# Performance work log

Hardware: AMD Instinct MI355X
Metric: run time of the kernel (lower is better)

The kernel has to match this reference:

```python
import jax, jax.numpy as jnp
import numpy as np

N_EMBD = 1024
N_HEAD = 16
HEAD_DIM = N_EMBD // N_HEAD
EPS = 1e-5


def _gelu_tanh(x):
    c = jnp.sqrt(jnp.asarray(2.0 / jnp.pi, x.dtype))
    return 0.5 * x * (1.0 + jnp.tanh(c * (x + 0.044715 * x ** 3)))


def _layernorm(x, scale, shift):
    # torch.var defaults to unbiased (ddof=1) -- replicate exactly
    mean = jnp.mean(x, axis=-1, keepdims=True)
    var = jnp.var(x, axis=-1, keepdims=True, ddof=1)
    return (x - mean) / jnp.sqrt(var + EPS) * scale + shift


def setup_inputs() -> dict:
    key = jax.random.key(0)
    ks = jax.random.split(key, 8)
    d, h = N_EMBD, 4 * N_EMBD
    s = 0.02
    return {
        "x": jax.random.normal(ks[0], (2, 2048, d), jnp.float32),
        "ln1_scale": jnp.ones((d,), jnp.float32),
        "ln1_shift": jnp.zeros((d,), jnp.float32),
        "wq": jax.random.normal(ks[1], (d, d), jnp.float32) * s,
        "wk": jax.random.normal(ks[2], (d, d), jnp.float32) * s,
        "wv": jax.random.normal(ks[3], (d, d), jnp.float32) * s,
        "w_out": jax.random.normal(ks[4], (d, d), jnp.float32) * s,
        "b_out": jnp.zeros((d,), jnp.float32),
        "ln2_scale": jnp.ones((d,), jnp.float32),
        "ln2_shift": jnp.zeros((d,), jnp.float32),
        "w1": jax.random.normal(ks[5], (d, h), jnp.float32) * s,
        "b1": jnp.zeros((h,), jnp.float32),
        "w2": jax.random.normal(ks[6], (h, d), jnp.float32) * s,
        "b2": jnp.zeros((d,), jnp.float32),
    }


def reference(x, ln1_scale, ln1_shift, wq, wk, wv, w_out, b_out,
              ln2_scale, ln2_shift, w1, b1, w2, b2):
    B, S, D = x.shape
    out = _layernorm(x, ln1_scale, ln1_shift)

    # qkv projections (no bias), split heads: [B, H, S, hd]
    q = (out @ wq).reshape(B, S, N_HEAD, HEAD_DIM).transpose(0, 2, 1, 3)
    k = (out @ wk).reshape(B, S, N_HEAD, HEAD_DIM).transpose(0, 2, 1, 3)
    v = (out @ wv).reshape(B, S, N_HEAD, HEAD_DIM).transpose(0, 2, 1, 3)

    scores = jnp.einsum("bhqd,bhkd->bhqk", q, k)
    causal = jnp.triu(jnp.ones((S, S), bool), k=1)
    # original masks BEFORE scaling; -inf / sqrt(d) is still -inf
    scores = jnp.where(causal, -jnp.inf, scores)
    weights = jax.nn.softmax(scores / jnp.sqrt(jnp.asarray(HEAD_DIM, scores.dtype)), axis=-1)
    ctx = jnp.einsum("bhqk,bhkd->bqhd", weights, v).reshape(B, S, D)
    attn_out = ctx @ w_out + b_out

    out = attn_out + x  # dropout is identity (rate 0)
    shortcut = out
    out = _layernorm(out, ln2_scale, ln2_shift)
    out = _gelu_tanh(out @ w1 + b1) @ w2 + b2
    return out + shortcut
```

## Files before the change

### kernel.cpp

```cpp
#include <hip/hip_runtime.h>
#include <stdint.h>
#include <math.h>

using bf16x8 = __attribute__((ext_vector_type(8))) short;
using f32x4  = __attribute__((ext_vector_type(4))) float;

__device__ __forceinline__ uint16_t f2b(float f) {
    union { float f; uint32_t i; } v; v.f = f;
    uint32_t r = v.i + 0x7fffu + ((v.i >> 16) & 1u);
    return (uint16_t)(r >> 16);
}
__device__ __forceinline__ float b2f(uint16_t u) {
    union { uint32_t i; float f; } v; v.i = ((uint32_t)u) << 16; return v.f;
}

typedef const __attribute__((address_space(1))) void gvoid;
typedef __attribute__((address_space(3))) void svoid;

__global__ __launch_bounds__(256) void fill_zero(float* __restrict__ o, int n) {
    int i = (blockIdx.x * 256 + threadIdx.x) * 4;
    if (i < n) *(float4*)(o + i) = make_float4(0.f, 0.f, 0.f, 0.f);
}

__global__ __launch_bounds__(256) void transpose_qkvo(
    const float* __restrict__ wq, const float* __restrict__ wk,
    const float* __restrict__ wv, const float* __restrict__ wo,
    uint16_t* __restrict__ wqkvT, uint16_t* __restrict__ woT)
{
    const int D = 1024;
    int z = blockIdx.z;
    const float* W = (z == 0) ? wq : (z == 1) ? wk : (z == 2) ? wv : wo;
    uint16_t* Wt = (z < 3) ? (wqkvT + (size_t)z * D * D) : woT;
    __shared__ uint16_t t[32][33];
    int n0 = blockIdx.x * 32, k0 = blockIdx.y * 32;
    int tx = threadIdx.x, ty = threadIdx.y;
    #pragma unroll
    for (int i = ty; i < 32; i += 8)
        t[i][tx] = f2b(W[(size_t)(k0 + i) * D + (n0 + tx)]);
    __syncthreads();
    #pragma unroll
    for (int i = ty; i < 32; i += 8)
        Wt[(size_t)(n0 + i) * D + (k0 + tx)] = t[tx][i];
}

__global__ __launch_bounds__(256) void transpose_f2b(
    const float* __restrict__ W, uint16_t* __restrict__ Wt, int K, int N)
{
    __shared__ uint16_t t[32][33];
    int n0 = blockIdx.x * 32, k0 = blockIdx.y * 32;
    int tx = threadIdx.x, ty = threadIdx.y;
    #pragma unroll
    for (int i = ty; i < 32; i += 8)
        t[i][tx] = f2b(W[(size_t)(k0 + i) * N + (n0 + tx)]);
    __syncthreads();
    #pragma unroll
    for (int i = ty; i < 32; i += 8)
        Wt[(size_t)(n0 + i) * K + (k0 + tx)] = t[tx][i];
}

__global__ __launch_bounds__(256) void ln_kernel(
    const float* __restrict__ src, const float* __restrict__ scale,
    const float* __restrict__ shift, uint16_t* __restrict__ out)
{
    const int D = 1024;
    int row = blockIdx.x, t = threadIdx.x;
    float4 f = *((const float4*)(src + (size_t)row * D) + t);
    float v[4] = {f.x, f.y, f.z, f.w};
    float s1 = v[0] + v[1] + v[2] + v[3];
    float s2 = v[0]*v[0] + v[1]*v[1] + v[2]*v[2] + v[3]*v[3];
    #pragma unroll
    for (int off = 32; off; off >>= 1) {
        s1 += __shfl_xor(s1, off);
        s2 += __shfl_xor(s2, off);
    }
    __shared__ float red[2][4];
    __shared__ float stat[2];
    int wid = t >> 6, lane = t & 63;
    if (lane == 0) { red[0][wid] = s1; red[1][wid] = s2; }
    __syncthreads();
    if (t == 0) {
        float S1 = red[0][0] + red[0][1] + red[0][2] + red[0][3];
        float S2 = red[1][0] + red[1][1] + red[1][2] + red[1][3];
        float mean = S1 / (float)D;
        float var  = fmaxf((S2 - mean * S1) / (float)(D - 1), 0.f);
        stat[0] = mean; stat[1] = rsqrtf(var + 1e-5f);
    }
    __syncthreads();
    float mean = stat[0], rstd = stat[1];
    float4 sc = *((const float4*)scale + t);
    float4 sh = *((const float4*)shift + t);
    uint16_t o[4];
    o[0] = f2b((v[0] - mean) * rstd * sc.x + sh.x);
    o[1] = f2b((v[1] - mean) * rstd * sc.y + sh.y);
    o[2] = f2b((v[2] - mean) * rstd * sc.z + sh.z);
    o[3] = f2b((v[3] - mean) * rstd * sc.w + sh.w);
    uint2 st;
    st.x = (uint32_t)o[0] | ((uint32_t)o[1] << 16);
    st.y = (uint32_t)o[2] | ((uint32_t)o[3] << 16);
    *(uint2*)(out + (size_t)row * D + t * 4) = st;
}

__global__ __launch_bounds__(256) void combine2(
    float* __restrict__ dst, const float* __restrict__ part0,
    const float* __restrict__ resid, const float* __restrict__ bias)
{
    const int D = 1024;
    size_t o = (size_t)blockIdx.x * D + threadIdx.x * 4;
    float4 a = *(float4*)(dst + o);
    float4 b = *(const float4*)(part0 + o);
    float4 c = *(const float4*)(resid + o);
    float4 bv = *((const float4*)bias + threadIdx.x);
    a.x += b.x + c.x + bv.x;
    a.y += b.y + c.y + bv.y;
    a.z += b.z + c.z + bv.z;
    a.w += b.w + c.w + bv.w;
    *(float4*)(dst + o) = a;
}

__global__ __launch_bounds__(256) void combine2ln(
    float* __restrict__ res1, const float* __restrict__ part0,
    const float* __restrict__ x, const float* __restrict__ bo,
    const float* __restrict__ scale, const float* __restrict__ shift,
    uint16_t* __restrict__ out)
{
    const int D = 1024;
    int row = blockIdx.x, t = threadIdx.x;
    size_t o = (size_t)row * D + t * 4;
    float4 a = *(float4*)(res1 + o);
    float4 b = *(const float4*)(part0 + o);
    float4 c = *(const float4*)(x + o);
    float4 bv = *((const float4*)bo + t);
    float v[4] = {a.x + b.x + c.x + bv.x, a.y + b.y + c.y + bv.y,
                  a.z + b.z + c.z + bv.z, a.w + b.w + c.w + bv.w};
    *(float4*)(res1 + o) = make_float4(v[0], v[1], v[2], v[3]);

    float s1 = v[0] + v[1] + v[2] + v[3];
    float s2 = v[0]*v[0] + v[1]*v[1] + v[2]*v[2] + v[3]*v[3];
    #pragma unroll
    for (int off = 32; off; off >>= 1) {
        s1 += __shfl_xor(s1, off);
        s2 += __shfl_xor(s2, off);
    }
    __shared__ float red[2][4];
    __shared__ float stat[2];
    int wid = t >> 6, lane = t & 63;
    if (lane == 0) { red[0][wid] = s1; red[1][wid] = s2; }
    __syncthreads();
    if (t == 0) {
        float S1 = red[0][0] + red[0][1] + red[0][2] + red[0][3];
        float S2 = red[1][0] + red[1][1] + red[1][2] + red[1][3];
        float mean = S1 / (float)D;
        float var  = fmaxf((S2 - mean * S1) / (float)(D - 1), 0.f);
        stat[0] = mean; stat[1] = rsqrtf(var + 1e-5f);
    }
    __syncthreads();
    float mean = stat[0], rstd = stat[1];
    float4 sc = *((const float4*)scale + t);
    float4 sh = *((const float4*)shift + t);
    uint16_t ob[4];
    ob[0] = f2b((v[0] - mean) * rstd * sc.x + sh.x);
    ob[1] = f2b((v[1] - mean) * rstd * sc.y + sh.y);
    ob[2] = f2b((v[2] - mean) * rstd * sc.z + sh.z);
    ob[3] = f2b((v[3] - mean) * rstd * sc.w + sh.w);
    uint2 st;
    st.x = (uint32_t)ob[0] | ((uint32_t)ob[1] << 16);
    st.y = (uint32_t)ob[2] | ((uint32_t)ob[3] << 16);
    *(uint2*)(out + (size_t)row * D + t * 4) = st;
}

template <int EPI>
__global__ __launch_bounds__(256) void gemm128(
    const uint16_t* __restrict__ A, const uint16_t* __restrict__ Bt,
    const float* __restrict__ bias, const float* __restrict__ resid,
    void* __restrict__ outp, void* __restrict__ out2,
    int M, int N, int K, int lda)
{
    __shared__ __align__(16) uint16_t As[2][128 * 32];
    __shared__ __align__(16) uint16_t Bs[2][128 * 32];
    int tid = threadIdx.x;
    int w = tid >> 6, l = tid & 63;
    int quad = l >> 4, ln = l & 15;

    int Nt = gridDim.x, Mt = gridDim.y;
    int L0 = blockIdx.y * Nt + blockIdx.x;
    int nb = Nt * Mt;
    int L = (L0 & 7) * (nb >> 3) + (L0 >> 3);
    const int GROUP = 8;
    int nig = GROUP * Nt;
    int gid = L / nig;
    int fm = gid * GROUP;
    int gsz = min(Mt - fm, GROUP);
    int rem = L - gid * nig;
    int pid_m = fm + rem % gsz;
    int pid_n = rem / gsz;
    int n0 = pid_n * 128, m0 = pid_m * 128;
    int kofs = (EPI == 5) ? blockIdx.z * K : 0;

    int mo = (w & 1) * 64, no = (w >> 1) * 64;
    int srow = l >> 2;
    int scol = (l & 3) * 8;

    f32x4 acc[4][4];
    #pragma unroll
    for (int mi = 0; mi < 4; ++mi)
        #pragma unroll
        for (int ni = 0; ni < 4; ++ni) acc[mi][ni] = (f32x4){0.f, 0.f, 0.f, 0.f};

    for (int k0 = 0; k0 < K; k0 += 64) {
        __syncthreads();
        #pragma unroll
        for (int p = 0; p < 2; ++p) {
            int arow = p * 64 + w * 16 + srow;
            int ldst = (p * 64 + w * 16) * 32;
            const uint16_t* ga = A  + (size_t)(m0 + arow) * lda + kofs + k0 + scol;
            const uint16_t* gb = Bt + (size_t)(n0 + arow) * lda + kofs + k0 + scol;
            #pragma unroll
            for (int s = 0; s < 2; ++s) {
                __builtin_amdgcn_global_load_lds(
                    (gvoid*)(ga + s * 32), (svoid*)(As[s] + ldst), 16, 0, 0);
                __builtin_amdgcn_global_load_lds(
                    (gvoid*)(gb + s * 32), (svoid*)(Bs[s] + ldst), 16, 0, 0);
            }
        }
        __syncthreads();

        #pragma unroll
        for (int s = 0; s < 2; ++s) {
            bf16x8 af[4], bf[4];
            #pragma unroll
            for (int i = 0; i < 4; ++i)
                af[i] = *(const bf16x8*)(As[s] + (mo + i * 16 + ln) * 32 + quad * 8);
            #pragma unroll
            for (int i = 0; i < 4; ++i)
                bf[i] = *(const bf16x8*)(Bs[s] + (no + i * 16 + ln) * 32 + quad * 8);
            #pragma unroll
            for (int mi = 0; mi < 4; ++mi)
                #pragma unroll
                for (int ni = 0; ni < 4; ++ni)
                    acc[mi][ni] = __builtin_amdgcn_mfma_f32_16x16x32_bf16(
                        af[mi], bf[ni], acc[mi][ni], 0, 0, 0);
        }
    }

    float* pout = (EPI == 5) ? (blockIdx.z ? (float*)out2 : (float*)outp) : (float*)outp;

    #pragma unroll
    for (int ni = 0; ni < 4; ++ni) {
        int col = n0 + no + ni * 16 + ln;
        if (EPI == 4 && col >= 2048) {
            int hh = (col - 2048) >> 6, d = (col - 2048) & 63;
            #pragma unroll
            for (int mi = 0; mi < 4; ++mi) {
                int tok = m0 + mo + mi * 16 + quad * 4;
                int bat = tok >> 11, s = tok & 2047;
                uint16_t pk[4];
                #pragma unroll
                for (int r = 0; r < 4; ++r) pk[r] = f2b(acc[mi][ni][r]);
                uint2 st;
                st.x = (uint32_t)pk[0] | ((uint32_t)pk[1] << 16);
                st.y = (uint32_t)pk[2] | ((uint32_t)pk[3] << 16);
                *(uint2*)((uint16_t*)out2 +
                          ((size_t)(bat * 16 + hh) * 64 + d) * 2048 + s) = st;
            }
            continue;
        }
        float bv = (EPI == 1 || EPI == 2) ? bias[col] : 0.f;
        #pragma unroll
        for (int mi = 0; mi < 4; ++mi) {
            #pragma unroll
            for (int r = 0; r < 4; ++r) {
                int row = m0 + mo + mi * 16 + quad * 4 + r;
                float vacc = acc[mi][ni][r] + bv;
                if (EPI == 1) {
                    size_t idx = (size_t)row * N + col;
                    ((float*)outp)[idx] = vacc + resid[idx];
                } else if (EPI == 5) {
                    pout[(size_t)row * N + col] = vacc;
                } else if (EPI == 2) {
                    float x = vacc;
                    float u = 0.7978845608028654f * (x + 0.044715f * x * x * x);
                    float g = x / (1.f + __expf(-2.f * u));
                    ((uint16_t*)outp)[(size_t)row * N + col] = f2b(g);
                } else {
                    float vs = (col < 1024) ? vacc * 0.125f : vacc;
                    ((uint16_t*)outp)[(size_t)(col >> 10) * M * 1024 +
                                      (size_t)row * 1024 + (col & 1023)] = f2b(vs);
                }
            }
        }
    }
}

__device__ __forceinline__ void attn_tile(
    const uint16_t* __restrict__ Kl, const uint16_t* __restrict__ Vl,
    uint16_t* __restrict__ Pw,
    bf16x8 qf0, bf16x8 qf1,
    float* l_r, f32x4* o_acc,
    int qw, int kv0, bool diag, int quad, int ln)
{
    const int LW = 72;
    f32x4 sf[4];
    #pragma unroll
    for (int nt2 = 0; nt2 < 4; ++nt2) {
        const uint16_t* kp = Kl + (nt2 * 16 + ln) * LW + quad * 8;
        bf16x8 k0 = *(const bf16x8*)(kp);
        bf16x8 k1 = *(const bf16x8*)(kp + 32);
        f32x4 z = {0.f, 0.f, 0.f, 0.f};
        z = __builtin_amdgcn_mfma_f32_16x16x32_bf16(qf0, k0, z, 0, 0, 0);
        z = __builtin_amdgcn_mfma_f32_16x16x32_bf16(qf1, k1, z, 0, 0, 0);
        sf[nt2] = z;
    }
    #pragma unroll
    for (int r = 0; r < 4; ++r) {
        float ps = 0.f;
        if (diag) {
            int qrow = qw + quad * 4 + r;
            #pragma unroll
            for (int nt2 = 0; nt2 < 4; ++nt2) {
                int kv = kv0 + nt2 * 16 + ln;
                float pv = (kv <= qrow) ? __expf(sf[nt2][r]) : 0.f;
                sf[nt2][r] = pv;
                ps += pv;
            }
        } else {
            #pragma unroll
            for (int nt2 = 0; nt2 < 4; ++nt2) {
                float pv = __expf(sf[nt2][r]);
                sf[nt2][r] = pv;
                ps += pv;
            }
        }
        ps += __shfl_xor(ps, 1);
        ps += __shfl_xor(ps, 2);
        ps += __shfl_xor(ps, 4);
        ps += __shfl_xor(ps, 8);
        l_r[r] += ps;
    }
    #pragma unroll
    for (int nt2 = 0; nt2 < 4; ++nt2) {
        int gl = nt2 * 2 + (ln >> 3);
        int off = ln & 7;
        #pragma unroll
        for (int r = 0; r < 4; ++r) {
            int row = quad * 4 + r;
            int p = gl ^ ((quad << 1) ^ r);
            Pw[row * 64 + p * 8 + off] = f2b(sf[nt2][r]);
        }
    }
    int swl = ((ln >> 2) << 1) ^ (ln & 3);
    int g0 = quad ^ swl;
    int g1 = (quad + 4) ^ swl;
    bf16x8 p0 = *(const bf16x8*)(Pw + ln * 64 + g0 * 8);
    bf16x8 p1 = *(const bf16x8*)(Pw + ln * 64 + g1 * 8);
    #pragma unroll
    for (int dt = 0; dt < 4; ++dt) {
        const uint16_t* vp = Vl + (dt * 16 + ln) * LW + quad * 8;
        bf16x8 v0 = *(const bf16x8*)(vp);
        bf16x8 v1 = *(const bf16x8*)(vp + 32);
        o_acc[dt] = __builtin_amdgcn_mfma_f32_16x16x32_bf16(p0, v0, o_acc[dt], 0, 0, 0);
        o_acc[dt] = __builtin_amdgcn_mfma_f32_16x16x32_bf16(p1, v1, o_acc[dt], 0, 0, 0);
    }
}

__global__ __launch_bounds__(256) void attn_flash(
    const uint16_t* __restrict__ Q,
    const uint16_t* __restrict__ K,
    const uint16_t* __restrict__ Vt,
    uint16_t* __restrict__ O,
    int B, int S, int H)
{
    const int D = 1024;
    const int LW = 72;
    __shared__ uint16_t Kl[64 * 72];
    __shared__ uint16_t Vl[64 * 72];
    __shared__ uint16_t Pl[64 * 64];

    int tid = threadIdx.x;
    int w = tid >> 6, l = tid & 63;
    int quad = l >> 4, ln = l & 15;

    int NT = S / 64;
    int qlo = blockIdx.x;
    int qhi = NT - 1 - qlo;
    int h = blockIdx.y, b = blockIdx.z;
    size_t rb = (size_t)b * S;

    int qwl = qlo * 64 + w * 16;
    int qwh = qhi * 64 + w * 16;

    const uint16_t* qpl = Q + (rb + qwl + ln) * D + h * 64 + quad * 8;
    bf16x8 ql0 = *(const bf16x8*)(qpl);
    bf16x8 ql1 = *(const bf16x8*)(qpl + 32);
    const uint16_t* qph = Q + (rb + qwh + ln) * D + h * 64 + quad * 8;
    bf16x8 qh0 = *(const bf16x8*)(qph);
    bf16x8 qh1 = *(const bf16x8*)(qph + 32);

    const uint16_t* Kbase = K + rb * D + h * 64;
    const uint16_t* Vbase = Vt + (size_t)(b * H + h) * 64 * S;
    uint16_t* Pw = Pl + w * 16 * 64;

    int sr0 = tid >> 3,         sc0 = (tid & 7) * 8;
    int sr1 = (256 + tid) >> 3, sc1 = ((256 + tid) & 7) * 8;

    float lL[4] = {0.f, 0.f, 0.f, 0.f};
    float lH[4] = {0.f, 0.f, 0.f, 0.f};
    f32x4 oL[4], oH[4];
    #pragma unroll
    for (int dt = 0; dt < 4; ++dt) {
        oL[dt] = (f32x4){0.f, 0.f, 0.f, 0.f};
        oH[dt] = (f32x4){0.f, 0.f, 0.f, 0.f};
    }

    uint4 kr0 = *(const uint4*)(Kbase + (size_t)sr0 * D + sc0);
    uint4 kr1 = *(const uint4*)(Kbase + (size_t)sr1 * D + sc1);
    uint4 vr0 = *(const uint4*)(Vbase + (size_t)sr0 * S + sc0);
    uint4 vr1 = *(const uint4*)(Vbase + (size_t)sr1 * S + sc1);

    for (int t = 0; t <= qhi; ++t) {
        __syncthreads();
        *(uint4*)(Kl + sr0 * LW + sc0) = kr0;
        *(uint4*)(Kl + sr1 * LW + sc1) = kr1;
        *(uint4*)(Vl + sr0 * LW + sc0) = vr0;
        *(uint4*)(Vl + sr1 * LW + sc1) = vr1;
        __syncthreads();
        if (t < qhi) {
            int kv1 = (t + 1) * 64;
            kr0 = *(const uint4*)(Kbase + (size_t)(kv1 + sr0) * D + sc0);
            kr1 = *(const uint4*)(Kbase + (size_t)(kv1 + sr1) * D + sc1);
            vr0 = *(const uint4*)(Vbase + (size_t)sr0 * S + kv1 + sc0);
            vr1 = *(const uint4*)(Vbase + (size_t)sr1 * S + kv1 + sc1);
        }
        int kv0 = t * 64;
        attn_tile(Kl, Vl, Pw, qh0, qh1, lH, oH, qwh, kv0, t == qhi, quad, ln);
        if (t <= qlo)
            attn_tile(Kl, Vl, Pw, ql0, ql1, lL, oL, qwl, kv0, t == qlo, quad, ln);
    }

    #pragma unroll
    for (int r = 0; r < 4; ++r) {
        float invH = 1.f / lH[r];
        float invL = 1.f / lL[r];
        uint16_t* oph = O + (rb + qwh + quad * 4 + r) * D + h * 64 + ln;
        uint16_t* opl = O + (rb + qwl + quad * 4 + r) * D + h * 64 + ln;
        #pragma unroll
        for (int dt = 0; dt < 4; ++dt) {
            oph[dt * 16] = f2b(oH[dt][r] * invH);
            opl[dt * 16] = f2b(oL[dt][r] * invL);
        }
    }
}

extern "C" void kernel_launch(void* const* d_in, const int* in_sizes, int n_in,
                              void* d_out, int out_size, void* d_ws, size_t ws_size,
                              hipStream_t stream)
{
    (void)in_sizes; (void)n_in;
    const int B = 2, S = 2048, D = 1024, H = 16, F = 4096;
    const int M = B * S;
    const size_t MB = 1u << 20;

    const float* x    = (const float*)d_in[0];
    const float* ln1s = (const float*)d_in[1];
    const float* ln1b = (const float*)d_in[2];
    const float* wq   = (const float*)d_in[3];
    const float* wk   = (const float*)d_in[4];
    const float* wv   = (const float*)d_in[5];
    const float* wo   = (const float*)d_in[6];
    const float* bo   = (const float*)d_in[7];
    const float* ln2s = (const float*)d_in[8];
    const float* ln2b = (const float*)d_in[9];
    const float* w1   = (const float*)d_in[10];
    const float* b1   = (const float*)d_in[11];
    const float* w2   = (const float*)d_in[12];
    const float* b2   = (const float*)d_in[13];

    if (ws_size < 56 * MB) {
        fill_zero<<<(out_size + 1023) / 1024, 256, 0, stream>>>((float*)d_out, out_size);
        return;
    }
    bool full = ws_size >= 72 * MB;

    char* base = (char*)d_ws;
    uint16_t* woT    = (uint16_t*)(base + 0 * MB);
    uint16_t* wqkvT  = (uint16_t*)(base + 2 * MB);
    uint16_t* ln1o   = (uint16_t*)(base + 8 * MB);
    uint16_t* qb     = (uint16_t*)(base + 16 * MB);
    uint16_t* vbT    = (uint16_t*)(base + 32 * MB);
    uint16_t* ctx    = (uint16_t*)(base + 40 * MB);
    uint16_t* kb     = (uint16_t*)(base + 24 * MB);
    uint16_t* w1T    = (uint16_t*)(base + 0 * MB);
    float*    res1   = (float*)   (base + (full ? 56 : 16) * MB);
    uint16_t* ln2o   = (uint16_t*)(base + (full ? 8 : 32) * MB);
    uint16_t* w2T    = (uint16_t*)(base + (full ? 16 : 40) * MB);
    uint16_t* h1     = (uint16_t*)(base + (full ? 24 : 48) * MB);
    float*    part0  = (float*)   (base + 0 * MB);
    float*    partP  = (float*)   (base + 8 * MB);

    dim3 tb(32, 8);
    transpose_qkvo<<<dim3(D / 32, D / 32, 4), tb, 0, stream>>>(
        wq, wk, wv, wo, wqkvT, woT);

    ln_kernel<<<M, 256, 0, stream>>>(x, ln1s, ln1b, ln1o);

    gemm128<4><<<dim3(3072 / 128, M / 128), 256, 0, stream>>>(
        ln1o, wqkvT, nullptr, nullptr, qb, vbT, M, 3072, D, D);

    attn_flash<<<dim3(S / 128, H, B), 256, 0, stream>>>(qb, kb, vbT, ctx, B, S, H);

    if (full) {
        gemm128<5><<<dim3(D / 128, M / 128, 2), 256, 0, stream>>>(
            ctx, woT, nullptr, nullptr, partP, res1, M, D, D / 2, D);
        combine2ln<<<M, 256, 0, stream>>>(res1, partP, x, bo, ln2s, ln2b, ln2o);
    } else {
        gemm128<1><<<dim3(D / 128, M / 128), 256, 0, stream>>>(
            ctx, woT, bo, x, res1, nullptr, M, D, D, D);
        ln_kernel<<<M, 256, 0, stream>>>(res1, ln2s, ln2b, ln2o);
    }

    transpose_f2b<<<dim3(F / 32, D / 32), tb, 0, stream>>>(w1, w1T, D, F);
    transpose_f2b<<<dim3(D / 32, F / 32), tb, 0, stream>>>(w2, w2T, F, D);

    if (full) {
        gemm128<2><<<dim3(F / 128, M / 128), 256, 0, stream>>>(
            ln2o, w1T, b1, nullptr, h1, nullptr, M, F, D, D);
        gemm128<5><<<dim3(D / 128, M / 128, 2), 256, 0, stream>>>(
            h1, w2T, nullptr, nullptr, part0, d_out, M, D, F / 2, F);
        combine2<<<M, 256, 0, stream>>>((float*)d_out, part0, res1, b2);
    } else {
        const int MH = M / 2;
        for (int half = 0; half < 2; ++half) {
            size_t ro = (size_t)half * MH;
            gemm128<2><<<dim3(F / 128, MH / 128), 256, 0, stream>>>(
                ln2o + ro * D, w1T, b1, nullptr, h1, nullptr, MH, F, D, D);
            gemm128<1><<<dim3(D / 128, MH / 128), 256, 0, stream>>>(
                h1, w2T, b2, res1 + ro * D, (float*)d_out + ro * D, nullptr, MH, D, F, F);
        }
    }
}
```

Before: 360.8 us.

## Double-buffer GEMM LDS tiles with XOR-swizzled layout to overlap loads and MFMA

Rewrites the gemm128 main loop to ping-pong between two 128x64 LDS buffers, issuing the global-to-LDS loads for the next K-tile before computing the current one. This is meant to hide global memory latency behind MFMA work. It also switches the LDS layout to 64-wide rows with an XOR swizzle to reduce bank conflicts on fragment reads. LDS use doubles to 64 KB per block, which may reduce occupancy. The loop assumes K/64 is even and has no tail handling for odd tile counts.

```diff
diff --git a/kernel.cpp b/kernel.cpp
--- a/kernel.cpp
+++ b/kernel.cpp
@@ -168,6 +168,46 @@
     *(uint2*)(out + (size_t)row * D + t * 4) = st;
 }
 
+__device__ __forceinline__ void stage128(
+    const uint16_t* __restrict__ A, const uint16_t* __restrict__ Bt,
+    uint16_t* As, uint16_t* Bs,
+    int m0, int n0, int lda, int kk, int w, int l)
+{
+    int srow = l >> 3;
+    int sc = ((l & 7) ^ srow) << 3;
+    #pragma unroll
+    for (int p = 0; p < 4; ++p) {
+        int rbase = w * 32 + p * 8;
+        const uint16_t* ga = A  + (size_t)(m0 + rbase + srow) * lda + kk + sc;
+        const uint16_t* gb = Bt + (size_t)(n0 + rbase + srow) * lda + kk + sc;
+        __builtin_amdgcn_global_load_lds((gvoid*)ga, (svoid*)(As + rbase * 64), 16, 0, 0);
+        __builtin_amdgcn_global_load_lds((gvoid*)gb, (svoid*)(Bs + rbase * 64), 16, 0, 0);
+    }
+}
+
+__device__ __forceinline__ void comp128(
+    const uint16_t* As, const uint16_t* Bs, f32x4 (&acc)[4][4],
+    int mo, int no, int quad, int ln, int sw)
+{
+    #pragma unroll
+    for (int s = 0; s < 2; ++s) {
+        int cc = ((s * 64 + quad * 16) ^ sw) >> 1;
+        bf16x8 af[4], bf[4];
+        #pragma unroll
+        for (int i = 0; i < 4; ++i)
+            af[i] = *(const bf16x8*)(As + (mo + i * 16 + ln) * 64 + cc);
+        #pragma unroll
+        for (int i = 0; i < 4; ++i)
+            bf[i] = *(const bf16x8*)(Bs + (no + i * 16 + ln) * 64 + cc);
+        #pragma unroll
+        for (int mi = 0; mi < 4; ++mi)
+            #pragma unroll
+            for (int ni = 0; ni < 4; ++ni)
+                acc[mi][ni] = __builtin_amdgcn_mfma_f32_16x16x32_bf16(
+                    af[mi], bf[ni], acc[mi][ni], 0, 0, 0);
+    }
+}
+
 template <int EPI>
 __global__ __launch_bounds__(256) void gemm128(
     const uint16_t* __restrict__ A, const uint16_t* __restrict__ Bt,
@@ -175,11 +215,14 @@
     void* __restrict__ outp, void* __restrict__ out2,
     int M, int N, int K, int lda)
 {
-    __shared__ __align__(16) uint16_t As[2][128 * 32];
-    __shared__ __align__(16) uint16_t Bs[2][128 * 32];
+    __shared__ __align__(16) uint16_t As0[128 * 64];
+    __shared__ __align__(16) uint16_t As1[128 * 64];
+    __shared__ __align__(16) uint16_t Bs0[128 * 64];
+    __shared__ __align__(16) uint16_t Bs1[128 * 64];
     int tid = threadIdx.x;
     int w = tid >> 6, l = tid & 63;
     int quad = l >> 4, ln = l & 15;
+    int sw = (ln & 7) << 4;
 
     int Nt = gridDim.x, Mt = gridDim.y;
     int L0 = blockIdx.y * Nt + blockIdx.x;
@@ -197,8 +240,6 @@
     int kofs = (EPI == 5) ? blockIdx.z * K : 0;
 
     int mo = (w & 1) * 64, no = (w >> 1) * 64;
-    int srow = l >> 2;
-    int scol = (l & 3) * 8;
 
     f32x4 acc[4][4];
     #pragma unroll
@@ -206,40 +247,18 @@
         #pragma unroll
         for (int ni = 0; ni < 4; ++ni) acc[mi][ni] = (f32x4){0.f, 0.f, 0.f, 0.f};
 
-    for (int k0 = 0; k0 < K; k0 += 64) {
+    int nk = K >> 6;
+    stage128(A, Bt, As0, Bs0, m0, n0, lda, kofs, w, l);
+    __syncthreads();
+
+    for (int t = 0; t + 2 <= nk; t += 2) {
+        stage128(A, Bt, As1, Bs1, m0, n0, lda, kofs + (t + 1) * 64, w, l);
+        comp128(As0, Bs0, acc, mo, no, quad, ln, sw);
         __syncthreads();
-        #pragma unroll
-        for (int p = 0; p < 2; ++p) {
-            int arow = p * 64 + w * 16 + srow;
-            int ldst = (p * 64 + w * 16) * 32;
-            const uint16_t* ga = A  + (size_t)(m0 + arow) * lda + kofs + k0 + scol;
-            const uint16_t* gb = Bt + (size_t)(n0 + arow) * lda + kofs + k0 + scol;
-            #pragma unroll
-            for (int s = 0; s < 2; ++s) {
-                __builtin_amdgcn_global_load_lds(
-                    (gvoid*)(ga + s * 32), (svoid*)(As[s] + ldst), 16, 0, 0);
-                __builtin_amdgcn_global_load_lds(
-                    (gvoid*)(gb + s * 32), (svoid*)(Bs[s] + ldst), 16, 0, 0);
-            }
-        }
-        __syncthreads();
-
-        #pragma unroll
-        for (int s = 0; s < 2; ++s) {
-            bf16x8 af[4], bf[4];
-            #pragma unroll
-            for (int i = 0; i < 4; ++i)
-                af[i] = *(const bf16x8*)(As[s] + (mo + i * 16 + ln) * 32 + quad * 8);
-            #pragma unroll
-            for (int i = 0; i < 4; ++i)
-                bf[i] = *(const bf16x8*)(Bs[s] + (no + i * 16 + ln) * 32 + quad * 8);
-            #pragma unroll
-            for (int mi = 0; mi < 4; ++mi)
-                #pragma unroll
-                for (int ni = 0; ni < 4; ++ni)
-                    acc[mi][ni] = __builtin_amdgcn_mfma_f32_16x16x32_bf16(
-                        af[mi], bf[ni], acc[mi][ni], 0, 0, 0);
-        }
+        if (t + 2 < nk)
+            stage128(A, Bt, As0, Bs0, m0, n0, lda, kofs + (t + 2) * 64, w, l);
+        comp128(As1, Bs1, acc, mo, no, quad, ln, sw);
+        if (t + 2 < nk) __syncthreads();
     }
 
     float* pout = (EPI == 5) ? (blockIdx.z ? (float*)out2 : (float*)outp) : (float*)outp;
```

Result: faster. 349.2 us (-3.2%).
